# Kernel tuning notes

Hardware: AMD Instinct MI355X
Metric: run time of the kernel (lower is better)

Reference implementation:

```python
import jax, jax.numpy as jnp
import numpy as np


def setup_inputs() -> dict:
    key = jax.random.key(0)
    ks = jax.random.split(key, 6)
    b, t, e = 8, 2048, 1024
    q = jax.random.normal(ks[0], (b, t, e), dtype=jnp.float32)
    k = jax.random.normal(ks[1], (b, t, e), dtype=jnp.float32)
    v = jax.random.normal(ks[2], (b, t, e), dtype=jnp.float32)
    # nn.Linear(emb, emb, bias=False) weights, stored as [out, in] like torch
    s = 1.0 / np.sqrt(e)
    Wq = jax.random.uniform(ks[3], (e, e), dtype=jnp.float32, minval=-s, maxval=s)
    Wk = jax.random.uniform(ks[4], (e, e), dtype=jnp.float32, minval=-s, maxval=s)
    Wv = jax.random.uniform(ks[5], (e, e), dtype=jnp.float32, minval=-s, maxval=s)
    return {"q": q, "k": k, "v": v, "Wq": Wq, "Wk": Wk, "Wv": Wv}


def reference(q, k, v, Wq, Wk, Wv):
    b, t_q, e = q.shape
    t_k = k.shape[1]
    scale = e ** 0.25  # each of Q and K divided by e^(1/4) -> combined 1/sqrt(e)
    queries = jnp.einsum('bte,fe->btf', q, Wq) / scale
    keys = jnp.einsum('bte,fe->btf', k, Wk) / scale
    values = jnp.einsum('bte,fe->btf', v, Wv)
    dot = jnp.einsum('bqe,bke->bqk', queries, keys)  # [b, t_q, t_k]
    # self.mask=True: mask_(dot, -inf, mask_diagonal=False) zeroes strictly-upper triangle
    causal = jnp.triu(jnp.ones((t_q, t_k), dtype=bool), k=1)  # True above diagonal
    dot = jnp.where(causal[None, :, :], -jnp.inf, dot)
    attn = jax.nn.softmax(dot, axis=2)
    out = jnp.einsum('bqk,bke->bqe', attn, values)
    return out
```

## Files before the change

kernel.cpp:

```cpp
#include <hip/hip_runtime.h>
#include <hip/hip_bf16.h>


typedef short short8 __attribute__((ext_vector_type(8)));
typedef float f32x4 __attribute__((ext_vector_type(4)));
typedef int   int4v __attribute__((ext_vector_type(4)));

static constexpr int B_ = 8;
static constexpr int T_ = 2048;
static constexpr int E_ = 1024;

__device__ __forceinline__ float bf2f(ushort u) {
    union { unsigned int i; float f; } x; x.i = ((unsigned int)u) << 16; return x.f;
}
__device__ __forceinline__ ushort f2bf(float f) {
    union { float f; unsigned int i; } x; x.f = f;
    unsigned int r = x.i + 0x7fffu + ((x.i >> 16) & 1u);
    return (ushort)(r >> 16);
}
__device__ __forceinline__ short8 cvt8(f32x4 a, f32x4 b) {
    short8 r;
    union { __hip_bfloat162 h; unsigned int u; } p;
    unsigned int* ru = (unsigned int*)&r;
    p.h = __float22bfloat162_rn(make_float2(a[0], a[1])); ru[0] = p.u;
    p.h = __float22bfloat162_rn(make_float2(a[2], a[3])); ru[1] = p.u;
    p.h = __float22bfloat162_rn(make_float2(b[0], b[1])); ru[2] = p.u;
    p.h = __float22bfloat162_rn(make_float2(b[2], b[3])); ru[3] = p.u;
    return r;
}

__device__ __forceinline__ void async16(const ushort* g, ushort* l) {
    __builtin_amdgcn_global_load_lds(
        (const __attribute__((address_space(1))) unsigned int*)g,
        (__attribute__((address_space(3))) unsigned int*)l, 16, 0, 0);
}
__device__ __forceinline__ void async16f(const float* g, float* l) {
    __builtin_amdgcn_global_load_lds(
        (const __attribute__((address_space(1))) unsigned int*)g,
        (__attribute__((address_space(3))) unsigned int*)l, 16, 0, 0);
}

__device__ __forceinline__ void gemm_tile64(const ushort* __restrict__ A, int lda,
                                            const ushort* __restrict__ Bm, int ldb,
                                            int ksteps, f32x4 (&acc)[4][4],
                                            ushort* As, ushort* Bs)
{
    const int tid = threadIdx.x, lane = tid & 63, wave = tid >> 6;
    const int wr = (wave >> 1) * 64, wc = (wave & 1) * 64;
    const int srow = lane >> 3;
    const int scol = ((lane & 7) ^ srow) * 8;
    const int frow = lane & 15, q4 = lane >> 4;

    for (int ks = 0; ks < ksteps; ++ks) {
        const int k0 = ks * 64;
        __syncthreads();
#pragma unroll
        for (int j = 0; j < 4; ++j) {
            const int c = wave * 4 + j;
            const int grow = c * 8 + srow;
            async16(A  + (size_t)grow * lda + k0 + scol, As + c * 512);
            async16(Bm + (size_t)grow * ldb + k0 + scol, Bs + c * 512);
        }
        __syncthreads();

        short8 af[4][2], bf[4][2];
#pragma unroll
        for (int i = 0; i < 4; ++i) {
            const int ra = wr + i * 16 + frow;
            const int rb = wc + i * 16 + frow;
            const int sw = frow & 7;
#pragma unroll
            for (int kk = 0; kk < 2; ++kk) {
                const int g = (kk * 4 + q4) ^ sw;
                af[i][kk] = *(const short8*)(As + ra * 64 + g * 8);
                bf[i][kk] = *(const short8*)(Bs + rb * 64 + g * 8);
            }
        }
#pragma unroll
        for (int kk = 0; kk < 2; ++kk)
#pragma unroll
            for (int mi = 0; mi < 4; ++mi)
#pragma unroll
                for (int ni = 0; ni < 4; ++ni)
                    acc[mi][ni] = __builtin_amdgcn_mfma_f32_16x16x32_bf16(
                        af[mi][kk], bf[ni][kk], acc[mi][ni], 0, 0, 0);
    }
}

__global__ __launch_bounds__(256)
void cvtW_kernel(const float* __restrict__ w0, const float* __restrict__ w1,
                 const float* __restrict__ w2, ushort* __restrict__ d)
{
    const float* s = blockIdx.y == 0 ? w0 : (blockIdx.y == 1 ? w1 : w2);
    ushort* dd = d + (size_t)blockIdx.y * E_ * E_;
    const int idx = (blockIdx.x * 256 + threadIdx.x) * 8;
    f32x4 a = *(const f32x4*)(s + idx);
    f32x4 b = *(const f32x4*)(s + idx + 4);
    *(short8*)(dd + idx) = cvt8(a, b);
}

__global__ __launch_bounds__(256, 2)
void proj_kernel(const float* __restrict__ q, const float* __restrict__ k,
                 const float* __restrict__ v, const ushort* __restrict__ Wb,
                 ushort* __restrict__ Q, ushort* __restrict__ Kp,
                 ushort* __restrict__ Vt)
{
    __shared__ float  Asf[128 * 64];
    __shared__ ushort Bs[128 * 64];

    const int bid = blockIdx.x;
    const int n   = (bid & 7) * 384 + (bid >> 3);
    const int z   = n >> 10;
    const int rem = n & 1023;
    const int by  = rem & 7;
    const int bx  = rem >> 3;

    const float* A = (z == 0 ? q : (z == 1 ? k : v)) + (size_t)bx * 128 * E_;
    const ushort* W = Wb + (size_t)z * E_ * E_ + (size_t)by * 128 * E_;

    const int tid = threadIdx.x, lane = tid & 63, wave = tid >> 6;
    const int wr = (wave >> 1) * 64, wc = (wave & 1) * 64;
    const int aRowIn = lane >> 4;
    const int bRowIn = lane >> 3;
    const int frow = lane & 15, q4 = lane >> 4;

    f32x4 acc[4][4];
#pragma unroll
    for (int i = 0; i < 4; ++i)
#pragma unroll
        for (int j = 0; j < 4; ++j) acc[i][j] = (f32x4){0.f, 0.f, 0.f, 0.f};

    for (int ks = 0; ks < E_ / 64; ++ks) {
        const int k0 = ks * 64;
        __syncthreads();
#pragma unroll
        for (int j = 0; j < 8; ++j) {
            const int c = wave * 8 + j;
            const int row = c * 4 + aRowIn;
            const int sg = (lane & 15) ^ (row & 7);
            async16f(A + (size_t)row * E_ + k0 + sg * 4, Asf + c * 256);
        }
#pragma unroll
        for (int j = 0; j < 4; ++j) {
            const int c = wave * 4 + j;
            const int row = c * 8 + bRowIn;
            const int sg = (lane & 7) ^ (row & 7);
            async16(W + (size_t)row * E_ + k0 + sg * 8, Bs + c * 512);
        }
        __syncthreads();

#pragma unroll
        for (int kk = 0; kk < 2; ++kk) {
            short8 af[4], bf[4];
#pragma unroll
            for (int i = 0; i < 4; ++i) {
                const int Ra = wr + i * 16 + frow;
                const int sw = frow & 7;
                const int g0 = (kk * 8 + q4 * 2) ^ sw;
                const int g1 = g0 ^ 1;
                f32x4 lo = *(const f32x4*)(Asf + Ra * 64 + g0 * 4);
                f32x4 hi = *(const f32x4*)(Asf + Ra * 64 + g1 * 4);
                af[i] = cvt8(lo, hi);
                const int Rb = wc + i * 16 + frow;
                const int gb = (kk * 4 + q4) ^ sw;
                bf[i] = *(const short8*)(Bs + Rb * 64 + gb * 8);
            }
#pragma unroll
            for (int mi = 0; mi < 4; ++mi)
#pragma unroll
                for (int ni = 0; ni < 4; ++ni)
                    acc[mi][ni] = __builtin_amdgcn_mfma_f32_16x16x32_bf16(
                        af[mi], bf[ni], acc[mi][ni], 0, 0, 0);
        }
    }

    const float scale = (z == 2) ? 1.0f : 0.17677669529663687f;
    if (z < 2) {
        ushort* D = (z == 0 ? Q : Kp);
#pragma unroll
        for (int mi = 0; mi < 4; ++mi)
#pragma unroll
            for (int r = 0; r < 4; ++r) {
                const int row = bx * 128 + wr + mi * 16 + (lane >> 4) * 4 + r;
#pragma unroll
                for (int ni = 0; ni < 4; ++ni) {
                    const int col = by * 128 + wc + ni * 16 + (lane & 15);
                    D[(size_t)row * E_ + col] = f2bf(acc[mi][ni][r] * scale);
                }
            }
    } else {
#pragma unroll
        for (int mi = 0; mi < 4; ++mi)
#pragma unroll
            for (int r = 0; r < 4; ++r) {
                const int rowg = bx * 128 + wr + mi * 16 + (lane >> 4) * 4 + r;
                const int bb = rowg >> 11, tl = rowg & 2047;
#pragma unroll
                for (int ni = 0; ni < 4; ++ni) {
                    const int col = by * 128 + wc + ni * 16 + (lane & 15);
                    Vt[(size_t)bb * E_ * T_ + (size_t)col * T_ + tl] = f2bf(acc[mi][ni][r]);
                }
            }
    }
}

__global__ __launch_bounds__(256, 2)
void score_kernel(const ushort* __restrict__ Q, const ushort* __restrict__ K,
                  ushort* __restrict__ S)
{
    __shared__ ushort As[128 * 64];
    __shared__ ushort Bs[128 * 64];
    const int b = blockIdx.y;
    const int t = (blockIdx.x & 7) * 17 + (blockIdx.x >> 3);
    int br = (int)((sqrtf(8.0f * t + 1.0f) - 1.0f) * 0.5f);
    while ((br + 1) * (br + 2) / 2 <= t) ++br;
    while (br * (br + 1) / 2 > t) --br;
    const int bc = t - br * (br + 1) / 2;

    const ushort* A  = Q + ((size_t)b * T_ + br * 128) * E_;
    const ushort* Bm = K + ((size_t)b * T_ + bc * 128) * E_;

    f32x4 acc[4][4];
#pragma unroll
    for (int i = 0; i < 4; ++i)
#pragma unroll
        for (int j = 0; j < 4; ++j) acc[i][j] = (f32x4){0.f, 0.f, 0.f, 0.f};

    gemm_tile64(A, E_, Bm, E_, E_ / 64, acc, As, Bs);

    const int lane = threadIdx.x & 63, wave = threadIdx.x >> 6;
    const int wr = (wave >> 1) * 64, wc = (wave & 1) * 64;
    ushort* Sb = S + (size_t)b * T_ * T_;
#pragma unroll
    for (int mi = 0; mi < 4; ++mi)
#pragma unroll
        for (int r = 0; r < 4; ++r) {
            const int row = br * 128 + wr + mi * 16 + (lane >> 4) * 4 + r;
#pragma unroll
            for (int ni = 0; ni < 4; ++ni) {
                const int col = bc * 128 + wc + ni * 16 + (lane & 15);
                float val = acc[mi][ni][r];
                if (col > row) val = -1e30f;
                Sb[(size_t)row * T_ + col] = f2bf(val);
            }
        }
}

__global__ __launch_bounds__(256)
void softmax_kernel(ushort* __restrict__ S)
{
    const int gr = blockIdx.x;
    const int b = gr >> 11, i = gr & 2047;
    ushort* row = S + (size_t)b * T_ * T_ + (size_t)i * T_;
    const int Lpad = ((i >> 7) + 1) * 128;
    const int tid = threadIdx.x, lane = tid & 63, wave = tid >> 6;
    __shared__ float red[4];

    const int j0 = tid * 8;
    const bool act = j0 < Lpad;
    float xv[8];
    if (act) {
        int4v dv = *(const int4v*)(row + j0);
        const ushort* u = (const ushort*)&dv;
#pragma unroll
        for (int t = 0; t < 8; ++t) xv[t] = bf2f(u[t]);
    }

    float m = -1e30f;
    if (act)
#pragma unroll
        for (int t = 0; t < 8; ++t) m = fmaxf(m, xv[t]);
#pragma unroll
    for (int o = 32; o; o >>= 1) m = fmaxf(m, __shfl_xor(m, o, 64));
    if (lane == 0) red[wave] = m;
    __syncthreads();
    m = fmaxf(fmaxf(red[0], red[1]), fmaxf(red[2], red[3]));
    __syncthreads();

    float s = 0.f;
    if (act)
#pragma unroll
        for (int t = 0; t < 8; ++t) { xv[t] = __expf(xv[t] - m); s += xv[t]; }
#pragma unroll
    for (int o = 32; o; o >>= 1) s += __shfl_xor(s, o, 64);
    if (lane == 0) red[wave] = s;
    __syncthreads();
    s = red[0] + red[1] + red[2] + red[3];
    const float inv = 1.0f / s;

    if (act) {
        int4v dv;
        ushort* u = (ushort*)&dv;
#pragma unroll
        for (int t = 0; t < 8; ++t) u[t] = f2bf(xv[t] * inv);
        *(int4v*)(row + j0) = dv;
    }
}

__global__ __launch_bounds__(256, 2)
void out_kernel(const ushort* __restrict__ P, const ushort* __restrict__ Vt,
                float* __restrict__ O)
{
    __shared__ ushort As[128 * 64];
    __shared__ ushort Bs[128 * 64];
    const int bc = blockIdx.x, b = blockIdx.z;
    const int br = (int)gridDim.y - 1 - (int)blockIdx.y;
    const ushort* A  = P  + (size_t)b * T_ * T_ + (size_t)(br * 128) * T_;
    const ushort* Bm = Vt + (size_t)b * E_ * T_ + (size_t)(bc * 128) * T_;
    const int ksteps = (br + 1) * 2;

    f32x4 acc[4][4];
#pragma unroll
    for (int i = 0; i < 4; ++i)
#pragma unroll
        for (int j = 0; j < 4; ++j) acc[i][j] = (f32x4){0.f, 0.f, 0.f, 0.f};

    gemm_tile64(A, T_, Bm, T_, ksteps, acc, As, Bs);

    const int lane = threadIdx.x & 63, wave = threadIdx.x >> 6;
    const int wr = (wave >> 1) * 64, wc = (wave & 1) * 64;
    float* Ob = O + (size_t)b * T_ * E_;
#pragma unroll
    for (int mi = 0; mi < 4; ++mi)
#pragma unroll
        for (int r = 0; r < 4; ++r) {
            const int row = br * 128 + wr + mi * 16 + (lane >> 4) * 4 + r;
#pragma unroll
            for (int ni = 0; ni < 4; ++ni) {
                const int col = bc * 128 + wc + ni * 16 + (lane & 15);
                Ob[(size_t)row * E_ + col] = acc[mi][ni][r];
            }
        }
}

extern "C" void kernel_launch(void* const* d_in, const int* in_sizes, int n_in,
                              void* d_out, int out_size, void* d_ws, size_t ws_size,
                              hipStream_t stream)
{
    const float* q  = (const float*)d_in[0];
    const float* k  = (const float*)d_in[1];
    const float* v  = (const float*)d_in[2];
    const float* Wq = (const float*)d_in[3];
    const float* Wk = (const float*)d_in[4];
    const float* Wv = (const float*)d_in[5];
    float* out = (float*)d_out;

    const size_t nQKV = (size_t)B_ * T_ * E_;
    const size_t nW   = (size_t)E_ * E_;
    ushort* Q  = (ushort*)d_ws;
    ushort* K  = Q + nQKV;
    ushort* Vt = K + nQKV;
    ushort* S  = Vt + nQKV;
    ushort* Wb = S;

    cvtW_kernel<<<dim3(nW / 2048, 3), 256, 0, stream>>>(Wq, Wk, Wv, Wb);
    proj_kernel<<<dim3(3072), 256, 0, stream>>>(q, k, v, Wb, Q, K, Vt);
    score_kernel<<<dim3(136, B_), 256, 0, stream>>>(Q, K, S);
    softmax_kernel<<<dim3(B_ * T_), 256, 0, stream>>>(S);
    out_kernel<<<dim3(E_ / 128, T_ / 128, B_), 256, 0, stream>>>(S, Vt, out);
}
```

Baseline: 482.7 us.

## Prefetch fp32 A tile into registers and store bf16 to LDS in projection

The projection kernel no longer async-copies fp32 activation tiles into shared memory and converts them per fragment. Each thread now register-prefetches the next k-tile of fp32 A during the MFMA loop, converts it to bf16 once and writes it to a smaller swizzled bf16 LDS buffer. This halves A's LDS footprint and lets occupancy rise to 4 blocks per CU. The trade-offs are extra registers for the prefetch buffer, a tighter register budget under the higher launch bound, and hand-placed waitcnt and barrier synchronisation.

```diff
diff --git a/kernel.cpp b/kernel.cpp
--- a/kernel.cpp
+++ b/kernel.cpp
@@ -34,11 +34,6 @@
         (const __attribute__((address_space(1))) unsigned int*)g,
         (__attribute__((address_space(3))) unsigned int*)l, 16, 0, 0);
 }
-__device__ __forceinline__ void async16f(const float* g, float* l) {
-    __builtin_amdgcn_global_load_lds(
-        (const __attribute__((address_space(1))) unsigned int*)g,
-        (__attribute__((address_space(3))) unsigned int*)l, 16, 0, 0);
-}
 
 __device__ __forceinline__ void gemm_tile64(const ushort* __restrict__ A, int lda,
                                             const ushort* __restrict__ Bm, int ldb,
@@ -99,13 +94,13 @@
     *(short8*)(dd + idx) = cvt8(a, b);
 }
 
-__global__ __launch_bounds__(256, 2)
+__global__ __launch_bounds__(256, 4)
 void proj_kernel(const float* __restrict__ q, const float* __restrict__ k,
                  const float* __restrict__ v, const ushort* __restrict__ Wb,
                  ushort* __restrict__ Q, ushort* __restrict__ Kp,
                  ushort* __restrict__ Vt)
 {
-    __shared__ float  Asf[128 * 64];
+    __shared__ ushort As[128 * 64];
     __shared__ ushort Bs[128 * 64];
 
     const int bid = blockIdx.x;
@@ -120,7 +115,8 @@
 
     const int tid = threadIdx.x, lane = tid & 63, wave = tid >> 6;
     const int wr = (wave >> 1) * 64, wc = (wave & 1) * 64;
-    const int aRowIn = lane >> 4;
+    const int ar = tid >> 1;
+    const int ah = tid & 1;
     const int bRowIn = lane >> 3;
     const int frow = lane & 15, q4 = lane >> 4;
 
@@ -130,16 +126,14 @@
 #pragma unroll
         for (int j = 0; j < 4; ++j) acc[i][j] = (f32x4){0.f, 0.f, 0.f, 0.f};
 
-    for (int ks = 0; ks < E_ / 64; ++ks) {
+    f32x4 areg[8];
+#pragma unroll
+    for (int j = 0; j < 8; ++j)
+        areg[j] = *(const f32x4*)(A + (size_t)ar * E_ + ah * 32 + j * 4);
+
+    const int nt = E_ / 64;
+    for (int ks = 0; ks < nt; ++ks) {
         const int k0 = ks * 64;
-        __syncthreads();
-#pragma unroll
-        for (int j = 0; j < 8; ++j) {
-            const int c = wave * 8 + j;
-            const int row = c * 4 + aRowIn;
-            const int sg = (lane & 15) ^ (row & 7);
-            async16f(A + (size_t)row * E_ + k0 + sg * 4, Asf + c * 256);
-        }
 #pragma unroll
         for (int j = 0; j < 4; ++j) {
             const int c = wave * 4 + j;
@@ -147,7 +141,20 @@
             const int sg = (lane & 7) ^ (row & 7);
             async16(W + (size_t)row * E_ + k0 + sg * 8, Bs + c * 512);
         }
+#pragma unroll
+        for (int jj = 0; jj < 4; ++jj) {
+            const int slot = (ah * 4 + jj) ^ (ar & 7);
+            *(short8*)(As + ar * 64 + slot * 8) = cvt8(areg[2 * jj], areg[2 * jj + 1]);
+        }
         __syncthreads();
+
+        if (ks + 1 < nt) {
+            const int k1 = k0 + 64;
+#pragma unroll
+            for (int j = 0; j < 8; ++j)
+                areg[j] = *(const f32x4*)(A + (size_t)ar * E_ + k1 + ah * 32 + j * 4);
+        }
+        __builtin_amdgcn_sched_barrier(0);
 
 #pragma unroll
         for (int kk = 0; kk < 2; ++kk) {
@@ -156,14 +163,10 @@
             for (int i = 0; i < 4; ++i) {
                 const int Ra = wr + i * 16 + frow;
                 const int sw = frow & 7;
-                const int g0 = (kk * 8 + q4 * 2) ^ sw;
-                const int g1 = g0 ^ 1;
-                f32x4 lo = *(const f32x4*)(Asf + Ra * 64 + g0 * 4);
-                f32x4 hi = *(const f32x4*)(Asf + Ra * 64 + g1 * 4);
-                af[i] = cvt8(lo, hi);
+                const int g = (kk * 4 + q4) ^ sw;
+                af[i] = *(const short8*)(As + Ra * 64 + g * 8);
                 const int Rb = wc + i * 16 + frow;
-                const int gb = (kk * 4 + q4) ^ sw;
-                bf[i] = *(const short8*)(Bs + Rb * 64 + gb * 8);
+                bf[i] = *(const short8*)(Bs + Rb * 64 + g * 8);
             }
 #pragma unroll
             for (int mi = 0; mi < 4; ++mi)
@@ -172,6 +175,9 @@
                     acc[mi][ni] = __builtin_amdgcn_mfma_f32_16x16x32_bf16(
                         af[mi], bf[ni], acc[mi][ni], 0, 0, 0);
         }
+        asm volatile("s_waitcnt lgkmcnt(0)" ::: "memory");
+        __builtin_amdgcn_s_barrier();
+        __builtin_amdgcn_sched_barrier(0);
     }
 
     const float scale = (z == 2) ? 1.0f : 0.17677669529663687f;
```

Result: slower. 627.2 us (+29.9%).

## Double-buffer LDS tiles with async prefetch in projection, score and output GEMMs

Applied to the files above, without the earlier changes.

Replaces the single-buffered load-sync-compute loop in the score and output GEMMs with a two-stage ping-pong pipeline. The next K tile is issued with global_load_lds while the current one feeds MFMAs, using explicit vmcnt/lgkmcnt waits and raw barriers. The projection kernel gets the same treatment with a K step of 32, new swizzles and a plain 3D grid in place of the remapped 1D block order. This is meant to hide global memory latency, at the cost of double the LDS per block (which may cut occupancy) and the loss of the L2-friendly block ordering in proj. The hand-written wait counts must match the number of loads issued per stage or the results go wrong.

```diff
diff --git a/kernel.cpp b/kernel.cpp
--- a/kernel.cpp
+++ b/kernel.cpp
@@ -9,6 +9,12 @@
 static constexpr int B_ = 8;
 static constexpr int T_ = 2048;
 static constexpr int E_ = 1024;
+
+#define WAITVM8  asm volatile("s_waitcnt vmcnt(8)" ::: "memory")
+#define WAITVM6  asm volatile("s_waitcnt vmcnt(6)" ::: "memory")
+#define WAITVM0  asm volatile("s_waitcnt vmcnt(0)" ::: "memory")
+#define WAITLGKM asm volatile("s_waitcnt lgkmcnt(0)" ::: "memory")
+#define BARRIER  { __builtin_amdgcn_s_barrier(); __builtin_amdgcn_sched_barrier(0); }
 
 __device__ __forceinline__ float bf2f(ushort u) {
     union { unsigned int i; float f; } x; x.i = ((unsigned int)u) << 16; return x.f;
@@ -40,10 +46,52 @@
         (__attribute__((address_space(3))) unsigned int*)l, 16, 0, 0);
 }
 
-__device__ __forceinline__ void gemm_tile64(const ushort* __restrict__ A, int lda,
+__device__ __forceinline__ void stage64(const ushort* __restrict__ A, int lda,
+                                        const ushort* __restrict__ Bm, int ldb,
+                                        int k0, ushort* As, ushort* Bs,
+                                        int wave, int srow, int scol)
+{
+#pragma unroll
+    for (int j = 0; j < 4; ++j) {
+        const int c = wave * 4 + j;
+        const int grow = c * 8 + srow;
+        async16(A  + (size_t)grow * lda + k0 + scol, As + c * 512);
+        async16(Bm + (size_t)grow * ldb + k0 + scol, Bs + c * 512);
+    }
+}
+
+__device__ __forceinline__ void compute64(const ushort* As, const ushort* Bs,
+                                          f32x4 (&acc)[4][4],
+                                          int wr, int wc, int frow, int q4)
+{
+    short8 af[4][2], bf[4][2];
+#pragma unroll
+    for (int i = 0; i < 4; ++i) {
+        const int ra = wr + i * 16 + frow;
+        const int rb = wc + i * 16 + frow;
+        const int sw = frow & 7;
+#pragma unroll
+        for (int kk = 0; kk < 2; ++kk) {
+            const int g = (kk * 4 + q4) ^ sw;
+            af[i][kk] = *(const short8*)(As + ra * 64 + g * 8);
+            bf[i][kk] = *(const short8*)(Bs + rb * 64 + g * 8);
+        }
+    }
+#pragma unroll
+    for (int kk = 0; kk < 2; ++kk)
+#pragma unroll
+        for (int mi = 0; mi < 4; ++mi)
+#pragma unroll
+            for (int ni = 0; ni < 4; ++ni)
+                acc[mi][ni] = __builtin_amdgcn_mfma_f32_16x16x32_bf16(
+                    af[mi][kk], bf[ni][kk], acc[mi][ni], 0, 0, 0);
+}
+
+__device__ __forceinline__ void gemm_pipe64(const ushort* __restrict__ A, int lda,
                                             const ushort* __restrict__ Bm, int ldb,
                                             int ksteps, f32x4 (&acc)[4][4],
-                                            ushort* As, ushort* Bs)
+                                            ushort* As0, ushort* Bs0,
+                                            ushort* As1, ushort* Bs1)
 {
     const int tid = threadIdx.x, lane = tid & 63, wave = tid >> 6;
     const int wr = (wave >> 1) * 64, wc = (wave & 1) * 64;
@@ -51,39 +99,25 @@
     const int scol = ((lane & 7) ^ srow) * 8;
     const int frow = lane & 15, q4 = lane >> 4;
 
-    for (int ks = 0; ks < ksteps; ++ks) {
-        const int k0 = ks * 64;
-        __syncthreads();
-#pragma unroll
-        for (int j = 0; j < 4; ++j) {
-            const int c = wave * 4 + j;
-            const int grow = c * 8 + srow;
-            async16(A  + (size_t)grow * lda + k0 + scol, As + c * 512);
-            async16(Bm + (size_t)grow * ldb + k0 + scol, Bs + c * 512);
+    stage64(A, lda, Bm, ldb, 0, As0, Bs0, wave, srow, scol);
+
+    for (int kt = 0; kt < ksteps; kt += 2) {
+        stage64(A, lda, Bm, ldb, (kt + 1) * 64, As1, Bs1, wave, srow, scol);
+        WAITVM8;
+        BARRIER;
+        compute64(As0, Bs0, acc, wr, wc, frow, q4);
+        WAITLGKM;
+        BARRIER;
+        if (kt + 2 < ksteps) {
+            stage64(A, lda, Bm, ldb, (kt + 2) * 64, As0, Bs0, wave, srow, scol);
+            WAITVM8;
+        } else {
+            WAITVM0;
         }
-        __syncthreads();
-
-        short8 af[4][2], bf[4][2];
-#pragma unroll
-        for (int i = 0; i < 4; ++i) {
-            const int ra = wr + i * 16 + frow;
-            const int rb = wc + i * 16 + frow;
-            const int sw = frow & 7;
-#pragma unroll
-            for (int kk = 0; kk < 2; ++kk) {
-                const int g = (kk * 4 + q4) ^ sw;
-                af[i][kk] = *(const short8*)(As + ra * 64 + g * 8);
-                bf[i][kk] = *(const short8*)(Bs + rb * 64 + g * 8);
-            }
-        }
-#pragma unroll
-        for (int kk = 0; kk < 2; ++kk)
-#pragma unroll
-            for (int mi = 0; mi < 4; ++mi)
-#pragma unroll
-                for (int ni = 0; ni < 4; ++ni)
-                    acc[mi][ni] = __builtin_amdgcn_mfma_f32_16x16x32_bf16(
-                        af[mi][kk], bf[ni][kk], acc[mi][ni], 0, 0, 0);
+        BARRIER;
+        compute64(As1, Bs1, acc, wr, wc, frow, q4);
+        WAITLGKM;
+        BARRIER;
     }
 }
 
@@ -105,23 +139,19 @@
                  ushort* __restrict__ Q, ushort* __restrict__ Kp,
                  ushort* __restrict__ Vt)
 {
-    __shared__ float  Asf[128 * 64];
-    __shared__ ushort Bs[128 * 64];
-
-    const int bid = blockIdx.x;
-    const int n   = (bid & 7) * 384 + (bid >> 3);
-    const int z   = n >> 10;
-    const int rem = n & 1023;
-    const int by  = rem & 7;
-    const int bx  = rem >> 3;
-
+    __shared__ float  Asf0[128 * 32], Asf1[128 * 32];
+    __shared__ ushort Bs0[128 * 32],  Bs1[128 * 32];
+
+    const int bx = blockIdx.x, by = blockIdx.y, z = blockIdx.z;
     const float* A = (z == 0 ? q : (z == 1 ? k : v)) + (size_t)bx * 128 * E_;
     const ushort* W = Wb + (size_t)z * E_ * E_ + (size_t)by * 128 * E_;
 
     const int tid = threadIdx.x, lane = tid & 63, wave = tid >> 6;
     const int wr = (wave >> 1) * 64, wc = (wave & 1) * 64;
-    const int aRowIn = lane >> 4;
-    const int bRowIn = lane >> 3;
+    const int sArow = lane >> 3;
+    const int sAcol = ((lane & 7) ^ sArow) * 4;
+    const int sBrow = lane >> 2;
+    const int sBcol = ((lane & 3) ^ ((lane >> 3) & 3)) * 8;
     const int frow = lane & 15, q4 = lane >> 4;
 
     f32x4 acc[4][4];
@@ -130,49 +160,70 @@
 #pragma unroll
         for (int j = 0; j < 4; ++j) acc[i][j] = (f32x4){0.f, 0.f, 0.f, 0.f};
 
-    for (int ks = 0; ks < E_ / 64; ++ks) {
-        const int k0 = ks * 64;
-        __syncthreads();
-#pragma unroll
-        for (int j = 0; j < 8; ++j) {
-            const int c = wave * 8 + j;
-            const int row = c * 4 + aRowIn;
-            const int sg = (lane & 15) ^ (row & 7);
-            async16f(A + (size_t)row * E_ + k0 + sg * 4, Asf + c * 256);
+#define PROJ_STAGE(k0, Asf, Bs)                                               \
+    {                                                                         \
+        _Pragma("unroll")                                                     \
+        for (int j = 0; j < 4; ++j) {                                         \
+            const int c = wave * 4 + j;                                       \
+            async16f(A + (size_t)(c * 8 + sArow) * E_ + (k0) + sAcol,         \
+                     (Asf) + c * 256);                                        \
+        }                                                                     \
+        _Pragma("unroll")                                                     \
+        for (int j = 0; j < 2; ++j) {                                         \
+            const int c = wave * 2 + j;                                       \
+            async16(W + (size_t)(c * 16 + sBrow) * E_ + (k0) + sBcol,         \
+                    (Bs) + c * 512);                                          \
+        }                                                                     \
+    }
+
+#define PROJ_COMPUTE(Asf, Bs)                                                 \
+    {                                                                         \
+        short8 af[4], bf[4];                                                  \
+        _Pragma("unroll")                                                     \
+        for (int i = 0; i < 4; ++i) {                                         \
+            const int R = wr + i * 16 + frow;                                 \
+            const int g0 = (q4 * 2) ^ (frow & 7);                             \
+            const int g1 = g0 ^ 1;                                            \
+            f32x4 lo = *(const f32x4*)((Asf) + R * 32 + g0 * 4);              \
+            f32x4 hi = *(const f32x4*)((Asf) + R * 32 + g1 * 4);              \
+            af[i] = cvt8(lo, hi);                                             \
+        }                                                                     \
+        _Pragma("unroll")                                                     \
+        for (int i = 0; i < 4; ++i) {                                         \
+            const int R = wc + i * 16 + frow;                                 \
+            const int g = q4 ^ ((frow >> 1) & 3);                             \
+            bf[i] = *(const short8*)((Bs) + R * 32 + g * 8);                  \
+        }                                                                     \
+        _Pragma("unroll")                                                     \
+        for (int mi = 0; mi < 4; ++mi)                                        \
+            _Pragma("unroll")                                                 \
+            for (int ni = 0; ni < 4; ++ni)                                    \
+                acc[mi][ni] = __builtin_amdgcn_mfma_f32_16x16x32_bf16(        \
+                    af[mi], bf[ni], acc[mi][ni], 0, 0, 0);                    \
+    }
+
+    PROJ_STAGE(0, Asf0, Bs0);
+    const int nt = E_ / 32;
+    for (int kt = 0; kt < nt; kt += 2) {
+        PROJ_STAGE((kt + 1) * 32, Asf1, Bs1);
+        WAITVM6;
+        BARRIER;
+        PROJ_COMPUTE(Asf0, Bs0);
+        WAITLGKM;
+        BARRIER;
+        if (kt + 2 < nt) {
+            PROJ_STAGE((kt + 2) * 32, Asf0, Bs0);
+            WAITVM6;
+        } else {
+            WAITVM0;
         }
-#pragma unroll
-        for (int j = 0; j < 4; ++j) {
-            const int c = wave * 4 + j;
-            const int row = c * 8 + bRowIn;
-            const int sg = (lane & 7) ^ (row & 7);
-            async16(W + (size_t)row * E_ + k0 + sg * 8, Bs + c * 512);
-        }
-        __syncthreads();
-
-#pragma unroll
-        for (int kk = 0; kk < 2; ++kk) {
-            short8 af[4], bf[4];
-#pragma unroll
-            for (int i = 0; i < 4; ++i) {
-                const int Ra = wr + i * 16 + frow;
-                const int sw = frow & 7;
-                const int g0 = (kk * 8 + q4 * 2) ^ sw;
-                const int g1 = g0 ^ 1;
-                f32x4 lo = *(const f32x4*)(Asf + Ra * 64 + g0 * 4);
-                f32x4 hi = *(const f32x4*)(Asf + Ra * 64 + g1 * 4);
-                af[i] = cvt8(lo, hi);
-                const int Rb = wc + i * 16 + frow;
-                const int gb = (kk * 4 + q4) ^ sw;
-                bf[i] = *(const short8*)(Bs + Rb * 64 + gb * 8);
-            }
-#pragma unroll
-            for (int mi = 0; mi < 4; ++mi)
-#pragma unroll
-                for (int ni = 0; ni < 4; ++ni)
-                    acc[mi][ni] = __builtin_amdgcn_mfma_f32_16x16x32_bf16(
-                        af[mi], bf[ni], acc[mi][ni], 0, 0, 0);
-        }
-    }
+        BARRIER;
+        PROJ_COMPUTE(Asf1, Bs1);
+        WAITLGKM;
+        BARRIER;
+    }
+#undef PROJ_STAGE
+#undef PROJ_COMPUTE
 
     const float scale = (z == 2) ? 1.0f : 0.17677669529663687f;
     if (z < 2) {
@@ -208,8 +259,8 @@
 void score_kernel(const ushort* __restrict__ Q, const ushort* __restrict__ K,
                   ushort* __restrict__ S)
 {
-    __shared__ ushort As[128 * 64];
-    __shared__ ushort Bs[128 * 64];
+    __shared__ ushort As0[128 * 64], Bs0[128 * 64];
+    __shared__ ushort As1[128 * 64], Bs1[128 * 64];
     const int b = blockIdx.y;
     const int t = (blockIdx.x & 7) * 17 + (blockIdx.x >> 3);
     int br = (int)((sqrtf(8.0f * t + 1.0f) - 1.0f) * 0.5f);
@@ -226,7 +277,7 @@
 #pragma unroll
         for (int j = 0; j < 4; ++j) acc[i][j] = (f32x4){0.f, 0.f, 0.f, 0.f};
 
-    gemm_tile64(A, E_, Bm, E_, E_ / 64, acc, As, Bs);
+    gemm_pipe64(A, E_, Bm, E_, E_ / 64, acc, As0, Bs0, As1, Bs1);
 
     const int lane = threadIdx.x & 63, wave = threadIdx.x >> 6;
     const int wr = (wave >> 1) * 64, wc = (wave & 1) * 64;
@@ -301,8 +352,8 @@
 void out_kernel(const ushort* __restrict__ P, const ushort* __restrict__ Vt,
                 float* __restrict__ O)
 {
-    __shared__ ushort As[128 * 64];
-    __shared__ ushort Bs[128 * 64];
+    __shared__ ushort As0[128 * 64], Bs0[128 * 64];
+    __shared__ ushort As1[128 * 64], Bs1[128 * 64];
     const int bc = blockIdx.x, b = blockIdx.z;
     const int br = (int)gridDim.y - 1 - (int)blockIdx.y;
     const ushort* A  = P  + (size_t)b * T_ * T_ + (size_t)(br * 128) * T_;
@@ -315,7 +366,7 @@
 #pragma unroll
         for (int j = 0; j < 4; ++j) acc[i][j] = (f32x4){0.f, 0.f, 0.f, 0.f};
 
-    gemm_tile64(A, T_, Bm, T_, ksteps, acc, As, Bs);
+    gemm_pipe64(A, T_, Bm, T_, ksteps, acc, As0, Bs0, As1, Bs1);
 
     const int lane = threadIdx.x & 63, wave = threadIdx.x >> 6;
     const int wr = (wave >> 1) * 64, wc = (wave & 1) * 64;
@@ -354,7 +405,7 @@
     ushort* Wb = S;
 
     cvtW_kernel<<<dim3(nW / 2048, 3), 256, 0, stream>>>(Wq, Wk, Wv, Wb);
-    proj_kernel<<<dim3(3072), 256, 0, stream>>>(q, k, v, Wb, Q, K, Vt);
+    proj_kernel<<<dim3(128, 8, 3), 256, 0, stream>>>(q, k, v, Wb, Q, K, Vt);
     score_kernel<<<dim3(136, B_), 256, 0, stream>>>(Q, K, S);
     softmax_kernel<<<dim3(B_ * T_), 256, 0, stream>>>(S);
     out_kernel<<<dim3(E_ / 128, T_ / 128, B_), 256, 0, stream>>>(S, Vt, out);
```

Result: slower. 503.6 us (+4.3%).
